# Kernel tuning notes

Hardware: AMD Instinct MI355X
Metric: run time of the kernel (lower is better)

## Reference

```python
import jax, jax.numpy as jnp
import numpy as np

BLOCK = 128  # fp8 block-quant block size (block_size = [128, 128])


def _dequant(w, s):
    # w: [E, O, I] fp8-simulated values; s: [E, O, I//BLOCK] per-block scales
    # (scale_inv already repeat_interleaved along the out dim by the module).
    E, O, I = w.shape
    nb = s.shape[-1]
    bs = I // nb
    return (w.reshape(E, O, nb, bs) * s[..., None]).reshape(E, O, I)


def setup_inputs() -> dict:
    key = jax.random.key(0)
    ks = jax.random.split(key, 8)
    B, S, H, I, E = 1, 512, 2048, 768, 16
    return {
        "hidden_states": jax.random.normal(ks[0], (B, S, H), jnp.float32),
        "gate_w": jax.random.normal(ks[1], (E, H), jnp.float32) * 0.02,
        "w1": jax.random.normal(ks[2], (E, I, H), jnp.float32),
        "w1_scale": jax.random.uniform(ks[3], (E, I, H // BLOCK), jnp.float32, 0.005, 0.02),
        "w3": jax.random.normal(ks[4], (E, I, H), jnp.float32),
        "w3_scale": jax.random.uniform(ks[5], (E, I, H // BLOCK), jnp.float32, 0.005, 0.02),
        "w2": jax.random.normal(ks[6], (E, H, I), jnp.float32),
        "w2_scale": jax.random.uniform(ks[7], (E, H, I // BLOCK), jnp.float32, 0.005, 0.02),
        "top_k": 2,
    }


def reference(hidden_states, gate_w, w1, w1_scale, w3, w3_scale, w2, w2_scale, top_k):
    B, S, H = hidden_states.shape
    x = hidden_states.reshape(-1, H)           # [T, H]
    T = x.shape[0]
    E = gate_w.shape[0]

    # Router: sigmoid scores, top-k, sum-normalization (norm_topk_prob=False)
    router_logits = x @ gate_w.T               # [T, E]
    scores = jax.nn.sigmoid(router_logits.astype(jnp.float32))
    top_w, top_i = jax.lax.top_k(scores, top_k)
    top_w = top_w / jnp.sum(top_w, axis=-1, keepdims=True)

    # Dense combine matrix [T, E] (top-k sparse in the real kernel)
    combine = jnp.zeros((T, E), x.dtype).at[jnp.arange(T)[:, None], top_i].add(
        top_w.astype(x.dtype))

    # Inline block dequantization of fp8 weights
    w1d = _dequant(w1, w1_scale)               # [E, I, H]
    w3d = _dequant(w3, w3_scale)               # [E, I, H]
    w2d = _dequant(w2, w2_scale)               # [E, H, I]

    # SwiGLU expert MLPs (grouped GEMM expressed densely over experts)
    g = jnp.einsum('th,eih->eti', x, w1d)      # gate proj
    u = jnp.einsum('th,eih->eti', x, w3d)      # up proj
    a = jax.nn.silu(g) * u                     # [E, T, I]
    expert_out = jnp.einsum('eti,ehi->eth', a, w2d)  # down proj [E, T, H]

    y = jnp.einsum('te,eth->th', combine, expert_out)
    return y.reshape(B, S, H)
```

## Files before the change

### kernel.cpp

```cpp
#include <hip/hip_runtime.h>
#include <math.h>

#define H 2048
#define II 768
#define TT 512
#define EE 16
#define BK 64

typedef float f32x4 __attribute__((ext_vector_type(4)));
typedef short s16x8 __attribute__((ext_vector_type(8)));
typedef unsigned short u16;
typedef u16 u16x4 __attribute__((ext_vector_type(4)));
typedef u16 u16x8 __attribute__((ext_vector_type(8)));

__device__ __forceinline__ u16 f2bf(float f) {
  unsigned int u = __float_as_uint(f);
  u += 0x7fffu + ((u >> 16) & 1u);
  return (u16)(u >> 16);
}

__global__ void router_kernel(const float* __restrict__ x, const float* __restrict__ gw,
                              int* __restrict__ counts, int* __restrict__ topi,
                              float* __restrict__ topw, int* __restrict__ pos) {
  int t = blockIdx.x;
  int tid = threadIdx.x;
  int wave = tid >> 6, lane = tid & 63;
  __shared__ float logits[EE];
  const float* xt = x + (size_t)t * H;
  for (int e = wave * 4; e < wave * 4 + 4; ++e) {
    const float* ge = gw + (size_t)e * H;
    float p = 0.f;
    for (int h = lane * 4; h < H; h += 64 * 4) {
      f32x4 xv = *(const f32x4*)(xt + h);
      f32x4 gv = *(const f32x4*)(ge + h);
      p += xv[0]*gv[0] + xv[1]*gv[1] + xv[2]*gv[2] + xv[3]*gv[3];
    }
    #pragma unroll
    for (int off = 32; off > 0; off >>= 1) p += __shfl_down(p, off);
    if (lane == 0) logits[e] = p;
  }
  __syncthreads();
  if (tid == 0) {
    float s[EE];
    #pragma unroll
    for (int e = 0; e < EE; ++e) s[e] = 1.f / (1.f + expf(-logits[e]));
    int i0 = 0;
    for (int e = 1; e < EE; ++e) if (s[e] > s[i0]) i0 = e;
    int i1 = -1;
    for (int e = 0; e < EE; ++e) {
      if (e == i0) continue;
      if (i1 < 0 || s[e] > s[i1]) i1 = e;
    }
    float w0 = s[i0], w1v = s[i1];
    float inv = 1.f / (w0 + w1v);
    w0 *= inv; w1v *= inv;
    topi[t*2+0] = i0; topi[t*2+1] = i1;
    topw[t*2+0] = w0; topw[t*2+1] = w1v;
    pos[t*2+0] = atomicAdd(&counts[i0], 1);
    pos[t*2+1] = atomicAdd(&counts[i1], 1);
  }
}

__global__ void prefix_kernel(const int* __restrict__ counts, int* __restrict__ base) {
  int s = 0;
  for (int e = 0; e < EE; ++e) { base[e] = s; s += counts[e]; }
  base[EE] = s;
}

__global__ void gather_kernel(const float* __restrict__ x, const int* __restrict__ topi,
                              const float* __restrict__ topw, const int* __restrict__ pos,
                              const int* __restrict__ base, u16* __restrict__ Xg,
                              int* __restrict__ tok_of, float* __restrict__ wt_of) {
  int t = blockIdx.x, slot = blockIdx.y;
  int e = topi[t*2 + slot];
  int row = base[e] + pos[t*2 + slot];
  if (threadIdx.x == 0) { tok_of[row] = t; wt_of[row] = topw[t*2 + slot]; }
  const float* xt = x + (size_t)t * H;
  u16* dst = Xg + (size_t)row * H;
  int h = threadIdx.x * 8;
  f32x4 v0 = *(const f32x4*)(xt + h);
  f32x4 v1 = *(const f32x4*)(xt + h + 4);
  u16x8 o;
  o[0]=f2bf(v0[0]); o[1]=f2bf(v0[1]); o[2]=f2bf(v0[2]); o[3]=f2bf(v0[3]);
  o[4]=f2bf(v1[0]); o[5]=f2bf(v1[1]); o[6]=f2bf(v1[2]); o[7]=f2bf(v1[3]);
  *(u16x8*)(dst + h) = o;
}

__global__ __launch_bounds__(256, 3) void gemm1_kernel(
    const u16* __restrict__ Xg,
    const float* __restrict__ w1, const float* __restrict__ w1s,
    const float* __restrict__ w3, const float* __restrict__ w3s,
    const int* __restrict__ counts, const int* __restrict__ base,
    float* __restrict__ slab) {
  const int nc = blockIdx.x >> 2, kc = blockIdx.x & 3;
  const int e = blockIdx.y;
  const int cnt = counts[e];
  if (cnt == 0) return;
  const int n0 = nc * 64;
  const int k0 = kc * 512;
  const int b0 = base[e];
  const int tid = threadIdx.x;
  const int lane = tid & 63;
  const int wv = tid >> 6;
  const int wm = wv >> 1, wn = wv & 1;

  __shared__ __align__(16) u16 As[128 * 64];
  __shared__ __align__(16) u16 Bs[2][64 * 64];

  const int rA  = tid >> 1;
  const int ch  = tid & 1;
  const int cqA = ch << 5;
  const int swzA = (rA & 7) << 3;
  const int matB = rA >> 6;
  const int rB   = rA & 63;
  const int swzB = (rB & 7) << 3;
  const float* wsrc = (matB ? w3 : w1) + ((size_t)e * II + n0 + rB) * H + k0 + ch * 32;
  const float* ssrc = (matB ? w3s : w1s) + ((size_t)e * II + n0 + rB) * (H / 128) + kc * 4;
  u16* bdst = &Bs[matB][rB * 64];

  const int rswz = (lane & 7) << 3;
  const int acol0 = (lane >> 4) << 3;

  float* dst = slab + (size_t)wn * 1024 * II;

  const int nmt = (cnt + 127) >> 7;
  for (int mt = 0; mt < nmt; ++mt) {
    const u16* asrc = Xg + (size_t)(b0 + mt * 128 + rA) * H + k0 + cqA;
    f32x4 acc[4][4] = {};
    s16x8 av[4]; f32x4 bv[8]; float sc;
    #pragma unroll
    for (int j = 0; j < 4; ++j) av[j] = *(const s16x8*)(asrc + j * 8);
    #pragma unroll
    for (int j = 0; j < 8; ++j) bv[j] = *(const f32x4*)(wsrc + j * 4);
    sc = ssrc[(ch * 32) >> 7];
    {
      #pragma unroll
      for (int j = 0; j < 4; ++j)
        *(s16x8*)(As + rA * 64 + ((cqA + j * 8) ^ swzA)) = av[j];
      #pragma unroll
      for (int j = 0; j < 4; ++j) {
        u16x8 ob;
        ob[0]=f2bf(bv[2*j][0]*sc); ob[1]=f2bf(bv[2*j][1]*sc);
        ob[2]=f2bf(bv[2*j][2]*sc); ob[3]=f2bf(bv[2*j][3]*sc);
        ob[4]=f2bf(bv[2*j+1][0]*sc); ob[5]=f2bf(bv[2*j+1][1]*sc);
        ob[6]=f2bf(bv[2*j+1][2]*sc); ob[7]=f2bf(bv[2*j+1][3]*sc);
        *(u16x8*)(bdst + ((ch * 32 + j * 8) ^ swzB)) = ob;
      }
    }
    __syncthreads();
    for (int t = 0; t < 512 / BK; ++t) {
      const bool notlast = (t + 1 < 512 / BK);
      if (notlast) {
        const int k1 = (t + 1) * BK;
        #pragma unroll
        for (int j = 0; j < 4; ++j) av[j] = *(const s16x8*)(asrc + k1 + j * 8);
        #pragma unroll
        for (int j = 0; j < 8; ++j) bv[j] = *(const f32x4*)(wsrc + k1 + j * 4);
        sc = ssrc[(k1 + ch * 32) >> 7];
      }
      #pragma unroll
      for (int ks = 0; ks < 2; ++ks) {
        const int ac = ks * 32 + acol0;
        s16x8 bf[4];
        #pragma unroll
        for (int nf = 0; nf < 4; ++nf) {
          const int brn = nf * 16 + (lane & 15);
          bf[nf] = *(const s16x8*)(Bs[wn] + brn * 64 + (ac ^ rswz));
        }
        #pragma unroll
        for (int mi = 0; mi < 4; ++mi) {
          const int arow = wm * 64 + mi * 16 + (lane & 15);
          s16x8 af = *(const s16x8*)(As + arow * 64 + (ac ^ rswz));
          #pragma unroll
          for (int nf = 0; nf < 4; ++nf)
            acc[mi][nf] = __builtin_amdgcn_mfma_f32_16x16x32_bf16(af, bf[nf], acc[mi][nf], 0, 0, 0);
        }
      }
      __syncthreads();
      if (notlast) {
        #pragma unroll
        for (int j = 0; j < 4; ++j)
          *(s16x8*)(As + rA * 64 + ((cqA + j * 8) ^ swzA)) = av[j];
        #pragma unroll
        for (int j = 0; j < 4; ++j) {
          u16x8 ob;
          ob[0]=f2bf(bv[2*j][0]*sc); ob[1]=f2bf(bv[2*j][1]*sc);
          ob[2]=f2bf(bv[2*j][2]*sc); ob[3]=f2bf(bv[2*j][3]*sc);
          ob[4]=f2bf(bv[2*j+1][0]*sc); ob[5]=f2bf(bv[2*j+1][1]*sc);
          ob[6]=f2bf(bv[2*j+1][2]*sc); ob[7]=f2bf(bv[2*j+1][3]*sc);
          *(u16x8*)(bdst + ((ch * 32 + j * 8) ^ swzB)) = ob;
        }
      }
      __syncthreads();
    }
    #pragma unroll
    for (int mi = 0; mi < 4; ++mi) {
      #pragma unroll
      for (int r4 = 0; r4 < 4; ++r4) {
        const int mrow = mt * 128 + wm * 64 + mi * 16 + ((lane >> 4) << 2) + r4;
        if (mrow < cnt) {
          #pragma unroll
          for (int nf = 0; nf < 4; ++nf)
            atomicAdd(dst + (size_t)(b0 + mrow) * II + n0 + nf * 16 + (lane & 15),
                      acc[mi][nf][r4]);
        }
      }
    }
  }
}

__global__ void silu_kernel(const float* __restrict__ slab, u16* __restrict__ Ag) {
  const size_t i = ((size_t)blockIdx.x * 256 + threadIdx.x) * 4;
  f32x4 g = *(const f32x4*)(slab + i);
  f32x4 u = *(const f32x4*)(slab + (size_t)1024 * II + i);
  u16x4 o;
  #pragma unroll
  for (int j = 0; j < 4; ++j) {
    float a = g[j] / (1.f + expf(-g[j])) * u[j];
    o[j] = f2bf(a);
  }
  *(u16x4*)(Ag + i) = o;
}

__global__ __launch_bounds__(256, 4) void gemm2_kernel(
    const u16* __restrict__ Ag,
    const float* __restrict__ w2, const float* __restrict__ w2s,
    const int* __restrict__ counts, const int* __restrict__ base,
    const int* __restrict__ tok_of, const float* __restrict__ wt_of,
    float* __restrict__ y) {
  const int nc = blockIdx.x >> 1, kc = blockIdx.x & 1;
  const int e = blockIdx.y;
  const int cnt = counts[e];
  if (cnt == 0) return;
  const int n0 = nc * 64;
  const int k0 = kc * 384;
  const int b0 = base[e];
  const int tid = threadIdx.x;
  const int lane = tid & 63;
  const int wv = tid >> 6;
  const int wm = wv >> 1, wn = wv & 1;

  __shared__ __align__(16) u16 As[128 * 64];
  __shared__ __align__(16) u16 Bs[64 * 64];

  const int rA  = tid >> 1;
  const int cqA = (tid & 1) << 5;
  const int swzA = (rA & 7) << 3;
  const int rB  = tid >> 2;
  const int cqB = (tid & 3) << 4;
  const int swzB = (rB & 7) << 3;
  const float* wsrc = w2 + ((size_t)e * H + n0 + rB) * II + k0 + cqB;
  const float* ssrc = w2s + ((size_t)e * H + n0 + rB) * (II / 128) + kc * 3;
  u16* bdst = &Bs[rB * 64];

  const int rswz = (lane & 7) << 3;
  const int acol0 = (lane >> 4) << 3;

  const int nmt = (cnt + 127) >> 7;
  for (int mt = 0; mt < nmt; ++mt) {
    const u16* asrc = Ag + (size_t)(b0 + mt * 128 + rA) * II + k0 + cqA;
    f32x4 acc[4][2] = {};
    s16x8 av[4]; f32x4 bv[4]; float sc;
    #pragma unroll
    for (int j = 0; j < 4; ++j) av[j] = *(const s16x8*)(asrc + j * 8);
    #pragma unroll
    for (int j = 0; j < 4; ++j) bv[j] = *(const f32x4*)(wsrc + j * 4);
    sc = ssrc[0];
    {
      #pragma unroll
      for (int j = 0; j < 4; ++j)
        *(s16x8*)(As + rA * 64 + ((cqA + j * 8) ^ swzA)) = av[j];
      #pragma unroll
      for (int j = 0; j < 2; ++j) {
        u16x8 ob;
        ob[0]=f2bf(bv[2*j][0]*sc); ob[1]=f2bf(bv[2*j][1]*sc);
        ob[2]=f2bf(bv[2*j][2]*sc); ob[3]=f2bf(bv[2*j][3]*sc);
        ob[4]=f2bf(bv[2*j+1][0]*sc); ob[5]=f2bf(bv[2*j+1][1]*sc);
        ob[6]=f2bf(bv[2*j+1][2]*sc); ob[7]=f2bf(bv[2*j+1][3]*sc);
        *(u16x8*)(bdst + ((cqB + j * 8) ^ swzB)) = ob;
      }
    }
    __syncthreads();
    for (int t = 0; t < 384 / BK; ++t) {
      const bool notlast = (t + 1 < 384 / BK);
      if (notlast) {
        const int k1 = (t + 1) * BK;
        #pragma unroll
        for (int j = 0; j < 4; ++j) av[j] = *(const s16x8*)(asrc + k1 + j * 8);
        #pragma unroll
        for (int j = 0; j < 4; ++j) bv[j] = *(const f32x4*)(wsrc + k1 + j * 4);
        sc = ssrc[(k1 >> 7)];
      }
      #pragma unroll
      for (int ks = 0; ks < 2; ++ks) {
        const int ac = ks * 32 + acol0;
        s16x8 bf[2];
        #pragma unroll
        for (int ni = 0; ni < 2; ++ni) {
          const int brn = wn * 32 + ni * 16 + (lane & 15);
          bf[ni] = *(const s16x8*)(Bs + brn * 64 + (ac ^ rswz));
        }
        #pragma unroll
        for (int mi = 0; mi < 4; ++mi) {
          const int arow = wm * 64 + mi * 16 + (lane & 15);
          s16x8 af = *(const s16x8*)(As + arow * 64 + (ac ^ rswz));
          acc[mi][0] = __builtin_amdgcn_mfma_f32_16x16x32_bf16(af, bf[0], acc[mi][0], 0, 0, 0);
          acc[mi][1] = __builtin_amdgcn_mfma_f32_16x16x32_bf16(af, bf[1], acc[mi][1], 0, 0, 0);
        }
      }
      __syncthreads();
      if (notlast) {
        #pragma unroll
        for (int j = 0; j < 4; ++j)
          *(s16x8*)(As + rA * 64 + ((cqA + j * 8) ^ swzA)) = av[j];
        #pragma unroll
        for (int j = 0; j < 2; ++j) {
          u16x8 ob;
          ob[0]=f2bf(bv[2*j][0]*sc); ob[1]=f2bf(bv[2*j][1]*sc);
          ob[2]=f2bf(bv[2*j][2]*sc); ob[3]=f2bf(bv[2*j][3]*sc);
          ob[4]=f2bf(bv[2*j+1][0]*sc); ob[5]=f2bf(bv[2*j+1][1]*sc);
          ob[6]=f2bf(bv[2*j+1][2]*sc); ob[7]=f2bf(bv[2*j+1][3]*sc);
          *(u16x8*)(bdst + ((cqB + j * 8) ^ swzB)) = ob;
        }
      }
      __syncthreads();
    }
    #pragma unroll
    for (int mi = 0; mi < 4; ++mi) {
      #pragma unroll
      for (int r4 = 0; r4 < 4; ++r4) {
        const int mrow = mt * 128 + wm * 64 + mi * 16 + ((lane >> 4) << 2) + r4;
        if (mrow < cnt) {
          const int grow = b0 + mrow;
          const int tk = tok_of[grow];
          const float wt = wt_of[grow];
          #pragma unroll
          for (int ni = 0; ni < 2; ++ni)
            atomicAdd(y + (size_t)tk * H + n0 + wn * 32 + ni * 16 + (lane & 15),
                      acc[mi][ni][r4] * wt);
        }
      }
    }
  }
}

extern "C" void kernel_launch(void* const* d_in, const int* in_sizes, int n_in,
                              void* d_out, int out_size, void* d_ws, size_t ws_size,
                              hipStream_t stream) {
  const float* x   = (const float*)d_in[0];
  const float* gw  = (const float*)d_in[1];
  const float* w1  = (const float*)d_in[2];
  const float* w1s = (const float*)d_in[3];
  const float* w3  = (const float*)d_in[4];
  const float* w3s = (const float*)d_in[5];
  const float* w2  = (const float*)d_in[6];
  const float* w2s = (const float*)d_in[7];
  float* y = (float*)d_out;

  char* ws = (char*)d_ws;
  int*   counts = (int*)(ws + 0);
  int*   basep  = (int*)(ws + 64);
  int*   topi   = (int*)(ws + 256);
  float* topw   = (float*)(ws + 256 + 4096);
  int*   pos    = (int*)(ws + 256 + 8192);
  int*   tok_of = (int*)(ws + 256 + 12288);
  float* wt_of  = (float*)(ws + 256 + 16384);
  u16*   Xg     = (u16*)(ws + 20736);
  u16*   Ag     = (u16*)(ws + 20736 + 4718592);
  float* slab   = (float*)(ws + 20736 + 4718592 + 1769472);

  hipMemsetAsync(counts, 0, 64, stream);
  hipMemsetAsync(y, 0, (size_t)out_size * sizeof(float), stream);
  hipMemsetAsync(slab, 0, (size_t)2 * 1024 * II * sizeof(float), stream);

  router_kernel<<<TT, 256, 0, stream>>>(x, gw, counts, topi, topw, pos);
  prefix_kernel<<<1, 1, 0, stream>>>(counts, basep);
  gather_kernel<<<dim3(TT, 2), 256, 0, stream>>>(x, topi, topw, pos, basep, Xg, tok_of, wt_of);
  gemm1_kernel<<<dim3(48, EE), 256, 0, stream>>>(Xg, w1, w1s, w3, w3s, counts, basep, slab);
  silu_kernel<<<(1024 * II) / (256 * 4), 256, 0, stream>>>(slab, Ag);
  gemm2_kernel<<<dim3(64, EE), 256, 0, stream>>>(Ag, w2, w2s, counts, basep, tok_of, wt_of, y);
}
```

Measured before the change: 150.3 us.

## Double-buffer LDS and prefetch two K-steps ahead in both expert GEMMs

Both grouped GEMM kernels now use double-buffered shared memory tiles with register prefetch issued two K-steps ahead, so each iteration needs one barrier instead of two. Block scales are hoisted into registers before the tile loop. This aims to hide global weight-load latency behind MFMA work and cut synchronisation. The cost is double the LDS footprint and more registers, so launch-bound occupancy targets are lowered (3→2 and 4→3), which may reduce concurrent blocks.

Measured after the change: 153.8 us. 1.02x slower.

```diff
diff --git a/kernel.cpp b/kernel.cpp
--- a/kernel.cpp
+++ b/kernel.cpp
@@ -86,7 +86,7 @@
   *(u16x8*)(dst + h) = o;
 }
 
-__global__ __launch_bounds__(256, 3) void gemm1_kernel(
+__global__ __launch_bounds__(256, 2) void gemm1_kernel(
     const u16* __restrict__ Xg,
     const float* __restrict__ w1, const float* __restrict__ w1s,
     const float* __restrict__ w3, const float* __restrict__ w3s,
@@ -104,8 +104,8 @@
   const int wv = tid >> 6;
   const int wm = wv >> 1, wn = wv & 1;
 
-  __shared__ __align__(16) u16 As[128 * 64];
-  __shared__ __align__(16) u16 Bs[2][64 * 64];
+  __shared__ __align__(16) u16 As[2][128 * 64];
+  __shared__ __align__(16) u16 Bs[2][2][64 * 64];
 
   const int rA  = tid >> 1;
   const int ch  = tid & 1;
@@ -116,7 +116,9 @@
   const int swzB = (rB & 7) << 3;
   const float* wsrc = (matB ? w3 : w1) + ((size_t)e * II + n0 + rB) * H + k0 + ch * 32;
   const float* ssrc = (matB ? w3s : w1s) + ((size_t)e * II + n0 + rB) * (H / 128) + kc * 4;
-  u16* bdst = &Bs[matB][rB * 64];
+  float scl[4];
+  #pragma unroll
+  for (int j = 0; j < 4; ++j) scl[j] = ssrc[j];
 
   const int rswz = (lane & 7) << 3;
   const int acol0 = (lane >> 4) << 3;
@@ -127,72 +129,63 @@
   for (int mt = 0; mt < nmt; ++mt) {
     const u16* asrc = Xg + (size_t)(b0 + mt * 128 + rA) * H + k0 + cqA;
     f32x4 acc[4][4] = {};
-    s16x8 av[4]; f32x4 bv[8]; float sc;
-    #pragma unroll
-    for (int j = 0; j < 4; ++j) av[j] = *(const s16x8*)(asrc + j * 8);
-    #pragma unroll
-    for (int j = 0; j < 8; ++j) bv[j] = *(const f32x4*)(wsrc + j * 4);
-    sc = ssrc[(ch * 32) >> 7];
-    {
-      #pragma unroll
-      for (int j = 0; j < 4; ++j)
-        *(s16x8*)(As + rA * 64 + ((cqA + j * 8) ^ swzA)) = av[j];
-      #pragma unroll
-      for (int j = 0; j < 4; ++j) {
-        u16x8 ob;
-        ob[0]=f2bf(bv[2*j][0]*sc); ob[1]=f2bf(bv[2*j][1]*sc);
-        ob[2]=f2bf(bv[2*j][2]*sc); ob[3]=f2bf(bv[2*j][3]*sc);
-        ob[4]=f2bf(bv[2*j+1][0]*sc); ob[5]=f2bf(bv[2*j+1][1]*sc);
-        ob[6]=f2bf(bv[2*j+1][2]*sc); ob[7]=f2bf(bv[2*j+1][3]*sc);
-        *(u16x8*)(bdst + ((ch * 32 + j * 8) ^ swzB)) = ob;
+    s16x8 av[2][4];
+    f32x4 bv[2][8];
+
+#define G1_ISSUE(t, P)                                                         \
+    { const int kk = (t) * BK;                                                 \
+      _Pragma("unroll") for (int j = 0; j < 4; ++j)                            \
+        av[P][j] = *(const s16x8*)(asrc + kk + j * 8);                         \
+      _Pragma("unroll") for (int j = 0; j < 8; ++j)                            \
+        bv[P][j] = *(const f32x4*)(wsrc + kk + j * 4); }
+
+#define G1_CONVW(t, P)                                                         \
+    { u16* abuf = &As[(t) & 1][0];                                             \
+      u16* bbuf = &Bs[(t) & 1][matB][0];                                       \
+      _Pragma("unroll") for (int j = 0; j < 4; ++j)                            \
+        *(s16x8*)(abuf + rA * 64 + ((cqA + j * 8) ^ swzA)) = av[P][j];         \
+      const float ss = scl[(t) >> 1];                                          \
+      _Pragma("unroll") for (int j = 0; j < 4; ++j) {                          \
+        u16x8 ob;                                                              \
+        ob[0]=f2bf(bv[P][2*j][0]*ss); ob[1]=f2bf(bv[P][2*j][1]*ss);            \
+        ob[2]=f2bf(bv[P][2*j][2]*ss); ob[3]=f2bf(bv[P][2*j][3]*ss);            \
+        ob[4]=f2bf(bv[P][2*j+1][0]*ss); ob[5]=f2bf(bv[P][2*j+1][1]*ss);        \
+        ob[6]=f2bf(bv[P][2*j+1][2]*ss); ob[7]=f2bf(bv[P][2*j+1][3]*ss);        \
+        *(u16x8*)(bbuf + rB * 64 + ((ch * 32 + j * 8) ^ swzB)) = ob; } }
+
+#define G1_MFMA(t)                                                             \
+    { const u16* abuf = &As[(t) & 1][0];                                       \
+      const u16* bbuf = &Bs[(t) & 1][wn][0];                                   \
+      _Pragma("unroll") for (int ks = 0; ks < 2; ++ks) {                       \
+        const int ac = ks * 32 + acol0;                                        \
+        s16x8 bf[4];                                                           \
+        _Pragma("unroll") for (int nf = 0; nf < 4; ++nf)                       \
+          bf[nf] = *(const s16x8*)(bbuf + (nf * 16 + (lane & 15)) * 64 + (ac ^ rswz)); \
+        _Pragma("unroll") for (int mi = 0; mi < 4; ++mi) {                     \
+          const int arow = wm * 64 + mi * 16 + (lane & 15);                    \
+          s16x8 af = *(const s16x8*)(abuf + arow * 64 + (ac ^ rswz));          \
+          _Pragma("unroll") for (int nf = 0; nf < 4; ++nf)                     \
+            acc[mi][nf] = __builtin_amdgcn_mfma_f32_16x16x32_bf16(af, bf[nf], acc[mi][nf], 0, 0, 0); } } }
+
+    G1_ISSUE(0, 0)
+    G1_ISSUE(1, 1)
+    G1_CONVW(0, 0)
+    asm volatile("s_waitcnt lgkmcnt(0)" ::: "memory");
+    __builtin_amdgcn_s_barrier();
+    #pragma unroll
+    for (int t = 0; t < 8; ++t) {
+      if (t + 2 < 8) { G1_ISSUE(t + 2, t & 1) }
+      G1_MFMA(t)
+      if (t + 1 < 8) {
+        G1_CONVW(t + 1, (t + 1) & 1)
+        asm volatile("s_waitcnt lgkmcnt(0)" ::: "memory");
+        __builtin_amdgcn_s_barrier();
       }
     }
-    __syncthreads();
-    for (int t = 0; t < 512 / BK; ++t) {
-      const bool notlast = (t + 1 < 512 / BK);
-      if (notlast) {
-        const int k1 = (t + 1) * BK;
-        #pragma unroll
-        for (int j = 0; j < 4; ++j) av[j] = *(const s16x8*)(asrc + k1 + j * 8);
-        #pragma unroll
-        for (int j = 0; j < 8; ++j) bv[j] = *(const f32x4*)(wsrc + k1 + j * 4);
-        sc = ssrc[(k1 + ch * 32) >> 7];
-      }
-      #pragma unroll
-      for (int ks = 0; ks < 2; ++ks) {
-        const int ac = ks * 32 + acol0;
-        s16x8 bf[4];
-        #pragma unroll
-        for (int nf = 0; nf < 4; ++nf) {
-          const int brn = nf * 16 + (lane & 15);
-          bf[nf] = *(const s16x8*)(Bs[wn] + brn * 64 + (ac ^ rswz));
-        }
-        #pragma unroll
-        for (int mi = 0; mi < 4; ++mi) {
-          const int arow = wm * 64 + mi * 16 + (lane & 15);
-          s16x8 af = *(const s16x8*)(As + arow * 64 + (ac ^ rswz));
-          #pragma unroll
-          for (int nf = 0; nf < 4; ++nf)
-            acc[mi][nf] = __builtin_amdgcn_mfma_f32_16x16x32_bf16(af, bf[nf], acc[mi][nf], 0, 0, 0);
-        }
-      }
-      __syncthreads();
-      if (notlast) {
-        #pragma unroll
-        for (int j = 0; j < 4; ++j)
-          *(s16x8*)(As + rA * 64 + ((cqA + j * 8) ^ swzA)) = av[j];
-        #pragma unroll
-        for (int j = 0; j < 4; ++j) {
-          u16x8 ob;
-          ob[0]=f2bf(bv[2*j][0]*sc); ob[1]=f2bf(bv[2*j][1]*sc);
-          ob[2]=f2bf(bv[2*j][2]*sc); ob[3]=f2bf(bv[2*j][3]*sc);
-          ob[4]=f2bf(bv[2*j+1][0]*sc); ob[5]=f2bf(bv[2*j+1][1]*sc);
-          ob[6]=f2bf(bv[2*j+1][2]*sc); ob[7]=f2bf(bv[2*j+1][3]*sc);
-          *(u16x8*)(bdst + ((ch * 32 + j * 8) ^ swzB)) = ob;
-        }
-      }
-      __syncthreads();
-    }
+#undef G1_ISSUE
+#undef G1_CONVW
+#undef G1_MFMA
+
     #pragma unroll
     for (int mi = 0; mi < 4; ++mi) {
       #pragma unroll
@@ -206,6 +199,7 @@
         }
       }
     }
+    if (mt + 1 < nmt) __builtin_amdgcn_s_barrier();
   }
 }
 
@@ -222,7 +216,7 @@
   *(u16x4*)(Ag + i) = o;
 }
 
-__global__ __launch_bounds__(256, 4) void gemm2_kernel(
+__global__ __launch_bounds__(256, 3) void gemm2_kernel(
     const u16* __restrict__ Ag,
     const float* __restrict__ w2, const float* __restrict__ w2s,
     const int* __restrict__ counts, const int* __restrict__ base,
@@ -240,8 +234,8 @@
   const int wv = tid >> 6;
   const int wm = wv >> 1, wn = wv & 1;
 
-  __shared__ __align__(16) u16 As[128 * 64];
-  __shared__ __align__(16) u16 Bs[64 * 64];
+  __shared__ __align__(16) u16 As[2][128 * 64];
+  __shared__ __align__(16) u16 Bs[2][64 * 64];
 
   const int rA  = tid >> 1;
   const int cqA = (tid & 1) << 5;
@@ -251,7 +245,9 @@
   const int swzB = (rB & 7) << 3;
   const float* wsrc = w2 + ((size_t)e * H + n0 + rB) * II + k0 + cqB;
   const float* ssrc = w2s + ((size_t)e * H + n0 + rB) * (II / 128) + kc * 3;
-  u16* bdst = &Bs[rB * 64];
+  float scl[3];
+  #pragma unroll
+  for (int j = 0; j < 3; ++j) scl[j] = ssrc[j];
 
   const int rswz = (lane & 7) << 3;
   const int acol0 = (lane >> 4) << 3;
@@ -260,71 +256,64 @@
   for (int mt = 0; mt < nmt; ++mt) {
     const u16* asrc = Ag + (size_t)(b0 + mt * 128 + rA) * II + k0 + cqA;
     f32x4 acc[4][2] = {};
-    s16x8 av[4]; f32x4 bv[4]; float sc;
-    #pragma unroll
-    for (int j = 0; j < 4; ++j) av[j] = *(const s16x8*)(asrc + j * 8);
-    #pragma unroll
-    for (int j = 0; j < 4; ++j) bv[j] = *(const f32x4*)(wsrc + j * 4);
-    sc = ssrc[0];
-    {
-      #pragma unroll
-      for (int j = 0; j < 4; ++j)
-        *(s16x8*)(As + rA * 64 + ((cqA + j * 8) ^ swzA)) = av[j];
-      #pragma unroll
-      for (int j = 0; j < 2; ++j) {
-        u16x8 ob;
-        ob[0]=f2bf(bv[2*j][0]*sc); ob[1]=f2bf(bv[2*j][1]*sc);
-        ob[2]=f2bf(bv[2*j][2]*sc); ob[3]=f2bf(bv[2*j][3]*sc);
-        ob[4]=f2bf(bv[2*j+1][0]*sc); ob[5]=f2bf(bv[2*j+1][1]*sc);
-        ob[6]=f2bf(bv[2*j+1][2]*sc); ob[7]=f2bf(bv[2*j+1][3]*sc);
-        *(u16x8*)(bdst + ((cqB + j * 8) ^ swzB)) = ob;
+    s16x8 av[2][4];
+    f32x4 bv[2][4];
+
+#define G2_ISSUE(t, P)                                                         \
+    { const int kk = (t) * BK;                                                 \
+      _Pragma("unroll") for (int j = 0; j < 4; ++j)                            \
+        av[P][j] = *(const s16x8*)(asrc + kk + j * 8);                         \
+      _Pragma("unroll") for (int j = 0; j < 4; ++j)                            \
+        bv[P][j] = *(const f32x4*)(wsrc + kk + j * 4); }
+
+#define G2_CONVW(t, P)                                                         \
+    { u16* abuf = &As[(t) & 1][0];                                             \
+      u16* bbuf = &Bs[(t) & 1][0];                                             \
+      _Pragma("unroll") for (int j = 0; j < 4; ++j)                            \
+        *(s16x8*)(abuf + rA * 64 + ((cqA + j * 8) ^ swzA)) = av[P][j];         \
+      const float ss = scl[(t) >> 1];                                          \
+      _Pragma("unroll") for (int j = 0; j < 2; ++j) {                          \
+        u16x8 ob;                                                              \
+        ob[0]=f2bf(bv[P][2*j][0]*ss); ob[1]=f2bf(bv[P][2*j][1]*ss);            \
+        ob[2]=f2bf(bv[P][2*j][2]*ss); ob[3]=f2bf(bv[P][2*j][3]*ss);            \
+        ob[4]=f2bf(bv[P][2*j+1][0]*ss); ob[5]=f2bf(bv[P][2*j+1][1]*ss);        \
+        ob[6]=f2bf(bv[P][2*j+1][2]*ss); ob[7]=f2bf(bv[P][2*j+1][3]*ss);        \
+        *(u16x8*)(bbuf + rB * 64 + ((cqB + j * 8) ^ swzB)) = ob; } }
+
+#define G2_MFMA(t)                                                             \
+    { const u16* abuf = &As[(t) & 1][0];                                       \
+      const u16* bbuf = &Bs[(t) & 1][0];                                       \
+      _Pragma("unroll") for (int ks = 0; ks < 2; ++ks) {                       \
+        const int ac = ks * 32 + acol0;                                        \
+        s16x8 bf[2];                                                           \
+        _Pragma("unroll") for (int ni = 0; ni < 2; ++ni) {                     \
+          const int brn = wn * 32 + ni * 16 + (lane & 15);                     \
+          bf[ni] = *(const s16x8*)(bbuf + brn * 64 + (ac ^ rswz)); }           \
+        _Pragma("unroll") for (int mi = 0; mi < 4; ++mi) {                     \
+          const int arow = wm * 64 + mi * 16 + (lane & 15);                    \
+          s16x8 af = *(const s16x8*)(abuf + arow * 64 + (ac ^ rswz));          \
+          acc[mi][0] = __builtin_amdgcn_mfma_f32_16x16x32_bf16(af, bf[0], acc[mi][0], 0, 0, 0); \
+          acc[mi][1] = __builtin_amdgcn_mfma_f32_16x16x32_bf16(af, bf[1], acc[mi][1], 0, 0, 0); } } }
+
+    G2_ISSUE(0, 0)
+    G2_ISSUE(1, 1)
+    G2_CONVW(0, 0)
+    asm volatile("s_waitcnt lgkmcnt(0)" ::: "memory");
+    __builtin_amdgcn_s_barrier();
+    #pragma unroll
+    for (int t = 0; t < 6; ++t) {
+      if (t + 2 < 6) { G2_ISSUE(t + 2, t & 1) }
+      G2_MFMA(t)
+      if (t + 1 < 6) {
+        G2_CONVW(t + 1, (t + 1) & 1)
+        asm volatile("s_waitcnt lgkmcnt(0)" ::: "memory");
+        __builtin_amdgcn_s_barrier();
       }
     }
-    __syncthreads();
-    for (int t = 0; t < 384 / BK; ++t) {
-      const bool notlast = (t + 1 < 384 / BK);
-      if (notlast) {
-        const int k1 = (t + 1) * BK;
-        #pragma unroll
-        for (int j = 0; j < 4; ++j) av[j] = *(const s16x8*)(asrc + k1 + j * 8);
-        #pragma unroll
-        for (int j = 0; j < 4; ++j) bv[j] = *(const f32x4*)(wsrc + k1 + j * 4);
-        sc = ssrc[(k1 >> 7)];
-      }
-      #pragma unroll
-      for (int ks = 0; ks < 2; ++ks) {
-        const int ac = ks * 32 + acol0;
-        s16x8 bf[2];
-        #pragma unroll
-        for (int ni = 0; ni < 2; ++ni) {
-          const int brn = wn * 32 + ni * 16 + (lane & 15);
-          bf[ni] = *(const s16x8*)(Bs + brn * 64 + (ac ^ rswz));
-        }
-        #pragma unroll
-        for (int mi = 0; mi < 4; ++mi) {
-          const int arow = wm * 64 + mi * 16 + (lane & 15);
-          s16x8 af = *(const s16x8*)(As + arow * 64 + (ac ^ rswz));
-          acc[mi][0] = __builtin_amdgcn_mfma_f32_16x16x32_bf16(af, bf[0], acc[mi][0], 0, 0, 0);
-          acc[mi][1] = __builtin_amdgcn_mfma_f32_16x16x32_bf16(af, bf[1], acc[mi][1], 0, 0, 0);
-        }
-      }
-      __syncthreads();
-      if (notlast) {
-        #pragma unroll
-        for (int j = 0; j < 4; ++j)
-          *(s16x8*)(As + rA * 64 + ((cqA + j * 8) ^ swzA)) = av[j];
-        #pragma unroll
-        for (int j = 0; j < 2; ++j) {
-          u16x8 ob;
-          ob[0]=f2bf(bv[2*j][0]*sc); ob[1]=f2bf(bv[2*j][1]*sc);
-          ob[2]=f2bf(bv[2*j][2]*sc); ob[3]=f2bf(bv[2*j][3]*sc);
-          ob[4]=f2bf(bv[2*j+1][0]*sc); ob[5]=f2bf(bv[2*j+1][1]*sc);
-          ob[6]=f2bf(bv[2*j+1][2]*sc); ob[7]=f2bf(bv[2*j+1][3]*sc);
-          *(u16x8*)(bdst + ((cqB + j * 8) ^ swzB)) = ob;
-        }
-      }
-      __syncthreads();
-    }
+#undef G2_ISSUE
+#undef G2_CONVW
+#undef G2_MFMA
+
     #pragma unroll
     for (int mi = 0; mi < 4; ++mi) {
       #pragma unroll
@@ -341,6 +330,7 @@
         }
       }
     }
+    if (mt + 1 < nmt) __builtin_amdgcn_s_barrier();
   }
 }
 
```
